# Performance work log

Hardware: AMD Instinct MI355X
Metric: run time of the kernel (lower is better)

The kernel has to match this reference:

```python
import jax, jax.numpy as jnp
import numpy as np

GAMMA, LMBD, EPS = 0.99, 0.95, 0.2
T, D, H, A = 262144, 128, 256, 8


def _mlp_gauss(x, W1, b1, Wmu, bmu, Wlv, blv):
    h = jnp.tanh(x @ W1 + b1)
    return h @ Wmu + bmu, h @ Wlv + blv  # mu, logvar: [T, A]


def _critic(x, Wc1, bc1, Wc2, bc2):
    h = jnp.tanh(x @ Wc1 + bc1)
    return h @ Wc2 + bc2  # [T, 1]


def setup_inputs() -> dict:
    key = jax.random.key(0)
    ks = jax.random.split(key, 12)
    s = 0.05  # small init scale for stable exp()/ratio
    return {
        "state": jax.random.normal(ks[0], (T, D), jnp.float32),
        "next_state": jax.random.normal(ks[1], (T, D), jnp.float32),
        "action": jax.random.normal(ks[2], (T, A), jnp.float32),
        "beta_log_prob": jax.random.normal(ks[3], (T, A), jnp.float32) * 0.1,
        "reward": jax.random.normal(ks[4], (T,), jnp.float32),
        "W1": jax.random.normal(ks[5], (D, H), jnp.float32) * s,
        "b1": jnp.zeros((H,), jnp.float32),
        "Wmu": jax.random.normal(ks[6], (H, A), jnp.float32) * s,
        "bmu": jnp.zeros((A,), jnp.float32),
        "Wlv": jax.random.normal(ks[7], (H, A), jnp.float32) * s,
        "blv": jnp.zeros((A,), jnp.float32),
        "Wc1": jax.random.normal(ks[8], (D, H), jnp.float32) * s,
        "bc1": jnp.zeros((H,), jnp.float32),
        "Wc2": jax.random.normal(ks[9], (H, 1), jnp.float32) * s,
        "bc2": jnp.zeros((1,), jnp.float32),
    }


def reference(state, next_state, action, beta_log_prob, reward,
              W1, b1, Wmu, bmu, Wlv, blv, Wc1, bc1, Wc2, bc2):
    # critic values
    value = _critic(state, Wc1, bc1, Wc2, bc2)            # [T, 1]
    v0 = value[:, 0]                                       # [T]
    v1 = _critic(next_state, Wc1, bc1, Wc2, bc2)[:, 0]     # [T]

    # GAE: reverse recurrence gae_t = delta_t + gamma*lambda*gae_{t+1}
    delta = reward + GAMMA * v1 - v0                       # [T]

    def step(g, d):
        g = d + GAMMA * LMBD * g
        return g, g

    _, gae_rev = jax.lax.scan(step, jnp.float32(0.0), delta[::-1])
    # torch code rebuilds each gae into a fresh Tensor -> returns are detached
    ret = jax.lax.stop_gradient(gae_rev[::-1][:, None])    # [T, 1]

    advantage = ret - value                                # [T, 1] (grad via value)
    a_hat = (advantage - advantage.mean()) / (jnp.std(advantage, ddof=1) + 1e-7)

    # pi log-prob of actions under Normal(mu, sqrt(exp(logvar)))
    mu, logvar = _mlp_gauss(state, W1, b1, Wmu, bmu, Wlv, blv)  # [T, A]
    log_2pi = jnp.float32(np.log(2.0 * np.pi))
    pi_lp = -0.5 * ((action - mu) ** 2) * jnp.exp(-logvar) - 0.5 * logvar - 0.5 * log_2pi

    ratio = jnp.exp(jnp.sum(pi_lp - jax.lax.stop_gradient(beta_log_prob),
                            axis=1, keepdims=True))        # [T, 1]

    actor_loss = -jnp.sum(jnp.minimum(ratio * a_hat,
                                      jnp.clip(ratio, 1.0 - EPS, 1.0 + EPS) * a_hat))
    critic_loss = jnp.sum(advantage ** 2)
    return actor_loss + critic_loss
```

## Files before the change

kernel.cpp:

```cpp
#include <hip/hip_runtime.h>

#define T_N   262144
#define D_IN  128
#define H_HID 256
#define A_DIM 8
#define GAMMA 0.99f
#define EPS_C 0.2f
#define C_GL  0.9405f
#define HALF_LOG_2PI 0.9189385332f

typedef __attribute__((ext_vector_type(8))) short short8;
typedef __attribute__((ext_vector_type(4))) float f32x4;

__device__ __forceinline__ unsigned short f2bf(float f) {
  unsigned int u = __float_as_uint(f);
  u += 0x7FFFu + ((u >> 16) & 1u);
  return (unsigned short)(u >> 16);
}
__device__ __forceinline__ float fast_tanh(float x) {
  x = fminf(10.f, fmaxf(-10.f, x));
  float e = __expf(2.f * x);
  return 1.f - 2.f * __builtin_amdgcn_rcpf(e + 1.f);
}

__global__ __launch_bounds__(256) void k_prep(
    const float* __restrict__ Wc1, const float* __restrict__ W1,
    const float* __restrict__ Wmu, const float* __restrict__ Wlv,
    unsigned short* __restrict__ Wc1T, unsigned short* __restrict__ W1T,
    unsigned short* __restrict__ H1) {
  int i = blockIdx.x * 256 + threadIdx.x;
  if (i < 32768) {
    int n = i >> 7, k = i & 127;
    Wc1T[i] = f2bf(Wc1[k * 256 + n]);
  } else if (i < 65536) {
    int j = i - 32768; int n = j >> 7, k = j & 127;
    W1T[j] = f2bf(W1[k * 256 + n]);
  } else if (i < 69632) {
    int j = i - 65536; int h = j >> 8, n = j & 255;
    H1[j] = (h < 8) ? f2bf(Wmu[n * 8 + h]) : f2bf(Wlv[n * 8 + (h - 8)]);
  }
}

__global__ __launch_bounds__(256, 4) void k_critic(
    const float* __restrict__ state, const float* __restrict__ next_state,
    const unsigned short* __restrict__ Wc1T,
    const float* __restrict__ bc1, const float* __restrict__ Wc2,
    const float* __restrict__ bc2,
    float* __restrict__ v0out, float* __restrict__ v1out) {
  const int job = blockIdx.y;
  const int r0  = blockIdx.x * 64;
  const int tid = threadIdx.x;
  const int lane = tid & 63;
  const int wv   = tid >> 6;
  const int c    = lane & 15;
  const int quad = lane >> 4;

  __shared__ unsigned short sh_x[64 * 136];
  __shared__ float sh_v[64 * 4];

  const float* X = job ? next_state : state;
  float* out = job ? v1out : v0out;

  {
    const float4* Xv = (const float4*)(X + r0 * D_IN);
#pragma unroll
    for (int it = 0; it < 8; ++it) {
      int f4 = tid + it * 256;
      int row = f4 >> 5, c4 = f4 & 31;
      float4 v = Xv[f4];
      ushort4 u;
      u.x = f2bf(v.x); u.y = f2bf(v.y); u.z = f2bf(v.z); u.w = f2bf(v.w);
      *(ushort4*)(&sh_x[row * 136 + c4 * 4]) = u;
    }
  }

  short8 bfrag[4][4];
  float bias_c[4], wc2_c[4];
#pragma unroll
  for (int ct = 0; ct < 4; ++ct) {
    int n = wv * 64 + ct * 16 + c;
    bias_c[ct] = bc1[n];
    wc2_c[ct]  = Wc2[n];
#pragma unroll
    for (int ki = 0; ki < 4; ++ki)
      bfrag[ct][ki] = *(const short8*)(Wc1T + n * 128 + ki * 32 + quad * 8);
  }
  __syncthreads();

#pragma unroll
  for (int rt = 0; rt < 4; ++rt) {
    f32x4 acc[4];
#pragma unroll
    for (int ct = 0; ct < 4; ++ct) acc[ct] = (f32x4){0.f, 0.f, 0.f, 0.f};
#pragma unroll
    for (int ki = 0; ki < 4; ++ki) {
      short8 a = *(const short8*)(&sh_x[(rt * 16 + c) * 136 + ki * 32 + quad * 8]);
#pragma unroll
      for (int ct = 0; ct < 4; ++ct)
        acc[ct] = __builtin_amdgcn_mfma_f32_16x16x32_bf16(a, bfrag[ct][ki], acc[ct], 0, 0, 0);
    }
#pragma unroll
    for (int r = 0; r < 4; ++r) {
      float p = 0.f;
#pragma unroll
      for (int ct = 0; ct < 4; ++ct)
        p += fast_tanh(acc[ct][r] + bias_c[ct]) * wc2_c[ct];
      p += __shfl_xor(p, 1);
      p += __shfl_xor(p, 2);
      p += __shfl_xor(p, 4);
      p += __shfl_xor(p, 8);
      if (c == 0) sh_v[(rt * 16 + quad * 4 + r) * 4 + wv] = p;
    }
  }
  __syncthreads();
  if (tid < 64) {
    out[r0 + tid] = sh_v[tid * 4] + sh_v[tid * 4 + 1] + sh_v[tid * 4 + 2] +
                    sh_v[tid * 4 + 3] + bc2[0];
  }
}

__global__ __launch_bounds__(256, 4) void k_actor(
    const float* __restrict__ state,
    const float* __restrict__ action, const float* __restrict__ beta_lp,
    const unsigned short* __restrict__ W1T, const unsigned short* __restrict__ H1,
    const float* __restrict__ b1, const float* __restrict__ bmu,
    const float* __restrict__ blv,
    float* __restrict__ ratio) {
  const int r0  = blockIdx.x * 32;
  const int tid = threadIdx.x;
  const int lane = tid & 63;
  const int wv   = tid >> 6;
  const int c    = lane & 15;
  const int quad = lane >> 4;

  __shared__ unsigned short sh_x[32 * 136];
  __shared__ unsigned short sh_h[32 * 264];
  __shared__ float sh_hb[2 * 32 * 16];

  {
    const float4* Xv = (const float4*)(state + r0 * D_IN);
#pragma unroll
    for (int it = 0; it < 4; ++it) {
      int f4 = tid + it * 256;
      int row = f4 >> 5, c4 = f4 & 31;
      float4 v = Xv[f4];
      ushort4 u;
      u.x = f2bf(v.x); u.y = f2bf(v.y); u.z = f2bf(v.z); u.w = f2bf(v.w);
      *(ushort4*)(&sh_x[row * 136 + c4 * 4]) = u;
    }
  }

  short8 bfrag[4][4];
  float bias_c[4];
#pragma unroll
  for (int ct = 0; ct < 4; ++ct) {
    int n = wv * 64 + ct * 16 + c;
    bias_c[ct] = b1[n];
#pragma unroll
    for (int ki = 0; ki < 4; ++ki)
      bfrag[ct][ki] = *(const short8*)(W1T + n * 128 + ki * 32 + quad * 8);
  }
  __syncthreads();

#pragma unroll
  for (int rt = 0; rt < 2; ++rt) {
    f32x4 acc[4];
#pragma unroll
    for (int ct = 0; ct < 4; ++ct) acc[ct] = (f32x4){0.f, 0.f, 0.f, 0.f};
#pragma unroll
    for (int ki = 0; ki < 4; ++ki) {
      short8 a = *(const short8*)(&sh_x[(rt * 16 + c) * 136 + ki * 32 + quad * 8]);
#pragma unroll
      for (int ct = 0; ct < 4; ++ct)
        acc[ct] = __builtin_amdgcn_mfma_f32_16x16x32_bf16(a, bfrag[ct][ki], acc[ct], 0, 0, 0);
    }
#pragma unroll
    for (int ct = 0; ct < 4; ++ct) {
      int col = wv * 64 + ct * 16 + c;
#pragma unroll
      for (int r = 0; r < 4; ++r) {
        int row = rt * 16 + quad * 4 + r;
        sh_h[row * 264 + col] = f2bf(fast_tanh(acc[ct][r] + bias_c[ct]));
      }
    }
  }
  __syncthreads();

  {
    const int st = wv & 1;
    const int kh = wv >> 1;
    f32x4 acc2 = (f32x4){0.f, 0.f, 0.f, 0.f};
#pragma unroll
    for (int kk = 0; kk < 4; ++kk) {
      int ki = kh * 4 + kk;
      short8 a2 = *(const short8*)(H1 + c * 256 + ki * 32 + quad * 8);
      short8 b2 = *(const short8*)(&sh_h[(st * 16 + c) * 264 + ki * 32 + quad * 8]);
      acc2 = __builtin_amdgcn_mfma_f32_16x16x32_bf16(a2, b2, acc2, 0, 0, 0);
    }
    *((f32x4*)&sh_hb[(kh * 32 + st * 16 + c) * 16 + quad * 4]) = acc2;
  }
  __syncthreads();

  {
    int s = tid >> 3, a = tid & 7;
    int t = r0 + s;
    float mu = sh_hb[(s)*16 + a] + sh_hb[(32 + s) * 16 + a] + bmu[a];
    float lv = sh_hb[(s)*16 + 8 + a] + sh_hb[(32 + s) * 16 + 8 + a] + blv[a];
    float ac = action[t * A_DIM + a];
    float bl = beta_lp[t * A_DIM + a];
    float d = ac - mu;
    float term = -0.5f * d * d * __expf(-lv) - 0.5f * lv - HALF_LOG_2PI - bl;
    term += __shfl_xor(term, 1);
    term += __shfl_xor(term, 2);
    term += __shfl_xor(term, 4);
    if (a == 0) ratio[t] = __expf(term);
  }
}

__global__ __launch_bounds__(256) void k_gae(
    const float* __restrict__ reward, const float* __restrict__ v0,
    const float* __restrict__ v1, float* __restrict__ adv,
    float* __restrict__ accs) {
  const int j = blockIdx.x, k = threadIdx.x;
  const int base = j * 1024 + k * 8;
  float d[8];
  float s = 0.f, w = 1.f;
#pragma unroll
  for (int i = 0; i < 8; ++i) {
    int idx = base + i;
    float dd = 0.f;
    if (idx < T_N) dd = reward[idx] + GAMMA * v1[idx] - v0[idx];
    d[i] = dd;
    s += w * dd;
    w *= C_GL;
  }
  const float W8 = w;
  __shared__ float Ss[256], Sw[256];
  Ss[k] = s; Sw[k] = W8;
  __syncthreads();
  for (int dd = 1; dd < 256; dd <<= 1) {
    bool has = (k + dd) < 256;
    float ns = 0.f, nw = 0.f;
    if (has) { ns = Ss[k] + Sw[k] * Ss[k + dd]; nw = Sw[k] * Sw[k + dd]; }
    __syncthreads();
    if (has) { Ss[k] = ns; Sw[k] = nw; }
    __syncthreads();
  }
  float g = (k < 255) ? Ss[k + 1] : 0.f;
  float sa = 0.f, sq = 0.f;
  if (k < 128) {
#pragma unroll
    for (int i = 7; i >= 0; --i) {
      g = d[i] + C_GL * g;
      float a = g - v0[base + i];
      adv[base + i] = a;
      sa += a; sq += a * a;
    }
  }
  __syncthreads();
  Ss[k] = sa; Sw[k] = sq;
  __syncthreads();
  for (int off = 128; off > 0; off >>= 1) {
    if (k < off) { Ss[k] += Ss[k + off]; Sw[k] += Sw[k + off]; }
    __syncthreads();
  }
  if (k == 0) {
    atomicAdd(&accs[0], Ss[0]);
    atomicAdd(&accs[1], Sw[0]);
  }
}

__global__ __launch_bounds__(256) void k_loss(
    const float* __restrict__ adv, const float* __restrict__ ratio,
    float* __restrict__ accs) {
  int t = blockIdx.x * 256 + threadIdx.x;
  float sum  = accs[0];
  float mean = sum * (1.f / (float)T_N);
  float var  = (accs[1] - sum * mean) / (float)(T_N - 1);
  float inv  = 1.f / (sqrtf(var) + 1e-7f);
  float a = (adv[t] - mean) * inv;
  float r = ratio[t];
  float rc = fminf(fmaxf(r, 1.f - EPS_C), 1.f + EPS_C);
  float term = -fminf(r * a, rc * a);
  __shared__ float red[256];
  int k = threadIdx.x;
  red[k] = term;
  __syncthreads();
  for (int off = 128; off > 0; off >>= 1) {
    if (k < off) red[k] += red[k + off];
    __syncthreads();
  }
  if (k == 0) atomicAdd(&accs[2], red[0]);
}

__global__ void k_fin(const float* __restrict__ accs, float* __restrict__ out) {
  out[0] = accs[2] + accs[1];
}

extern "C" void kernel_launch(void* const* d_in, const int* in_sizes, int n_in,
                              void* d_out, int out_size, void* d_ws, size_t ws_size,
                              hipStream_t stream) {
  const float* state      = (const float*)d_in[0];
  const float* next_state = (const float*)d_in[1];
  const float* action     = (const float*)d_in[2];
  const float* beta_lp    = (const float*)d_in[3];
  const float* reward     = (const float*)d_in[4];
  const float* W1   = (const float*)d_in[5];
  const float* b1   = (const float*)d_in[6];
  const float* Wmu  = (const float*)d_in[7];
  const float* bmu  = (const float*)d_in[8];
  const float* Wlv  = (const float*)d_in[9];
  const float* blv  = (const float*)d_in[10];
  const float* Wc1  = (const float*)d_in[11];
  const float* bc1  = (const float*)d_in[12];
  const float* Wc2  = (const float*)d_in[13];
  const float* bc2  = (const float*)d_in[14];

  char* ws = (char*)d_ws;
  size_t o = 0;
  unsigned short* Wc1T = (unsigned short*)(ws + o); o += 65536;
  unsigned short* W1T  = (unsigned short*)(ws + o); o += 65536;
  unsigned short* H1   = (unsigned short*)(ws + o); o += 8192;
  float* v0    = (float*)(ws + o); o += (size_t)T_N * 4;
  float* v1    = (float*)(ws + o); o += (size_t)T_N * 4;
  float* ratio = (float*)(ws + o); o += (size_t)T_N * 4;
  float* adv   = (float*)(ws + o); o += (size_t)T_N * 4;
  float* accs  = (float*)(ws + o); o += 256;

  hipMemsetAsync(accs, 0, 16, stream);

  k_prep<<<272, 256, 0, stream>>>(Wc1, W1, Wmu, Wlv, Wc1T, W1T, H1);

  dim3 gcrit(T_N / 64, 2);
  k_critic<<<gcrit, 256, 0, stream>>>(state, next_state, Wc1T, bc1, Wc2, bc2,
                                      v0, v1);
  k_actor<<<T_N / 32, 256, 0, stream>>>(state, action, beta_lp, W1T, H1,
                                        b1, bmu, blv, ratio);
  k_gae<<<256, 256, 0, stream>>>(reward, v0, v1, adv, accs);
  k_loss<<<T_N / 256, 256, 0, stream>>>(adv, ratio, accs);
  k_fin<<<1, 1, 0, stream>>>(accs, (float*)d_out);
}
```

Measured before the change: 440.4 us.

## Make critic/actor blocks persistent over multiple tiles with register prefetch; fold final kernel

Critic and actor kernels now loop over several 32-row tiles per block. Weight fragments are loaded into registers once per block, and the next tile's state rows are prefetched into registers while MFMA work runs on the current tile. The actor's second GEMM is split across all four waves by K, with a four-way partial-sum reduction. The separate finalize kernel is replaced by a last-block-done atomic counter inside k_loss. This cuts repeated weight loads and one launch, at the cost of fewer blocks and less parallelism across the grid.

```diff
diff --git a/kernel.cpp b/kernel.cpp
--- a/kernel.cpp
+++ b/kernel.cpp
@@ -8,6 +8,8 @@
 #define EPS_C 0.2f
 #define C_GL  0.9405f
 #define HALF_LOG_2PI 0.9189385332f
+#define CR_TPB 16
+#define AC_TPB 8
 
 typedef __attribute__((ext_vector_type(8))) short short8;
 typedef __attribute__((ext_vector_type(4))) float f32x4;
@@ -47,32 +49,14 @@
     const float* __restrict__ bc1, const float* __restrict__ Wc2,
     const float* __restrict__ bc2,
     float* __restrict__ v0out, float* __restrict__ v1out) {
-  const int job = blockIdx.y;
-  const int r0  = blockIdx.x * 64;
   const int tid = threadIdx.x;
   const int lane = tid & 63;
   const int wv   = tid >> 6;
   const int c    = lane & 15;
   const int quad = lane >> 4;
 
-  __shared__ unsigned short sh_x[64 * 136];
-  __shared__ float sh_v[64 * 4];
-
-  const float* X = job ? next_state : state;
-  float* out = job ? v1out : v0out;
-
-  {
-    const float4* Xv = (const float4*)(X + r0 * D_IN);
-#pragma unroll
-    for (int it = 0; it < 8; ++it) {
-      int f4 = tid + it * 256;
-      int row = f4 >> 5, c4 = f4 & 31;
-      float4 v = Xv[f4];
-      ushort4 u;
-      u.x = f2bf(v.x); u.y = f2bf(v.y); u.z = f2bf(v.z); u.w = f2bf(v.w);
-      *(ushort4*)(&sh_x[row * 136 + c4 * 4]) = u;
-    }
-  }
+  __shared__ unsigned short sh_x[32 * 136];
+  __shared__ float sh_v[32 * 4];
 
   short8 bfrag[4][4];
   float bias_c[4], wc2_c[4];
@@ -85,37 +69,73 @@
     for (int ki = 0; ki < 4; ++ki)
       bfrag[ct][ki] = *(const short8*)(Wc1T + n * 128 + ki * 32 + quad * 8);
   }
-  __syncthreads();
-
-#pragma unroll
-  for (int rt = 0; rt < 4; ++rt) {
-    f32x4 acc[4];
-#pragma unroll
-    for (int ct = 0; ct < 4; ++ct) acc[ct] = (f32x4){0.f, 0.f, 0.f, 0.f};
-#pragma unroll
-    for (int ki = 0; ki < 4; ++ki) {
-      short8 a = *(const short8*)(&sh_x[(rt * 16 + c) * 136 + ki * 32 + quad * 8]);
-#pragma unroll
-      for (int ct = 0; ct < 4; ++ct)
-        acc[ct] = __builtin_amdgcn_mfma_f32_16x16x32_bf16(a, bfrag[ct][ki], acc[ct], 0, 0, 0);
-    }
-#pragma unroll
-    for (int r = 0; r < 4; ++r) {
-      float p = 0.f;
-#pragma unroll
-      for (int ct = 0; ct < 4; ++ct)
-        p += fast_tanh(acc[ct][r] + bias_c[ct]) * wc2_c[ct];
-      p += __shfl_xor(p, 1);
-      p += __shfl_xor(p, 2);
-      p += __shfl_xor(p, 4);
-      p += __shfl_xor(p, 8);
-      if (c == 0) sh_v[(rt * 16 + quad * 4 + r) * 4 + wv] = p;
-    }
-  }
-  __syncthreads();
-  if (tid < 64) {
-    out[r0 + tid] = sh_v[tid * 4] + sh_v[tid * 4 + 1] + sh_v[tid * 4 + 2] +
-                    sh_v[tid * 4 + 3] + bc2[0];
+  const float vbias = bc2[0];
+
+  const int t0 = blockIdx.x * CR_TPB;
+
+  float4 rbuf[4];
+  {
+    const float* X = (t0 >> 13) ? next_state : state;
+    const float4* Xv = (const float4*)(X + (t0 & 8191) * 32 * D_IN);
+#pragma unroll
+    for (int j = 0; j < 4; ++j) rbuf[j] = Xv[tid + j * 256];
+  }
+
+  for (int i = 0; i < CR_TPB; ++i) {
+    const int T = t0 + i;
+    const int job = T >> 13;
+    const int r0  = (T & 8191) * 32;
+
+#pragma unroll
+    for (int j = 0; j < 4; ++j) {
+      int e = tid + j * 256;
+      int row = e >> 5, c4 = e & 31;
+      ushort4 u;
+      u.x = f2bf(rbuf[j].x); u.y = f2bf(rbuf[j].y);
+      u.z = f2bf(rbuf[j].z); u.w = f2bf(rbuf[j].w);
+      *(ushort4*)(&sh_x[row * 136 + c4 * 4]) = u;
+    }
+    __syncthreads();
+
+    if (i + 1 < CR_TPB) {
+      int T2 = T + 1;
+      const float* X2 = (T2 >> 13) ? next_state : state;
+      const float4* Xv2 = (const float4*)(X2 + (T2 & 8191) * 32 * D_IN);
+#pragma unroll
+      for (int j = 0; j < 4; ++j) rbuf[j] = Xv2[tid + j * 256];
+    }
+
+#pragma unroll
+    for (int rt = 0; rt < 2; ++rt) {
+      f32x4 acc[4];
+#pragma unroll
+      for (int ct = 0; ct < 4; ++ct) acc[ct] = (f32x4){0.f, 0.f, 0.f, 0.f};
+#pragma unroll
+      for (int ki = 0; ki < 4; ++ki) {
+        short8 a = *(const short8*)(&sh_x[(rt * 16 + c) * 136 + ki * 32 + quad * 8]);
+#pragma unroll
+        for (int ct = 0; ct < 4; ++ct)
+          acc[ct] = __builtin_amdgcn_mfma_f32_16x16x32_bf16(a, bfrag[ct][ki], acc[ct], 0, 0, 0);
+      }
+#pragma unroll
+      for (int r = 0; r < 4; ++r) {
+        float p = 0.f;
+#pragma unroll
+        for (int ct = 0; ct < 4; ++ct)
+          p += fast_tanh(acc[ct][r] + bias_c[ct]) * wc2_c[ct];
+        p += __shfl_xor(p, 1);
+        p += __shfl_xor(p, 2);
+        p += __shfl_xor(p, 4);
+        p += __shfl_xor(p, 8);
+        if (c == 0) sh_v[(rt * 16 + quad * 4 + r) * 4 + wv] = p;
+      }
+    }
+    __syncthreads();
+    if (tid < 32) {
+      float* out = job ? v1out : v0out;
+      out[r0 + tid] = sh_v[tid * 4] + sh_v[tid * 4 + 1] + sh_v[tid * 4 + 2] +
+                      sh_v[tid * 4 + 3] + vbias;
+    }
   }
 }
 
@@ -126,7 +146,6 @@
     const float* __restrict__ b1, const float* __restrict__ bmu,
     const float* __restrict__ blv,
     float* __restrict__ ratio) {
-  const int r0  = blockIdx.x * 32;
   const int tid = threadIdx.x;
   const int lane = tid & 63;
   const int wv   = tid >> 6;
@@ -135,20 +154,7 @@
 
   __shared__ unsigned short sh_x[32 * 136];
   __shared__ unsigned short sh_h[32 * 264];
-  __shared__ float sh_hb[2 * 32 * 16];
-
-  {
-    const float4* Xv = (const float4*)(state + r0 * D_IN);
-#pragma unroll
-    for (int it = 0; it < 4; ++it) {
-      int f4 = tid + it * 256;
-      int row = f4 >> 5, c4 = f4 & 31;
-      float4 v = Xv[f4];
-      ushort4 u;
-      u.x = f2bf(v.x); u.y = f2bf(v.y); u.z = f2bf(v.z); u.w = f2bf(v.w);
-      *(ushort4*)(&sh_x[row * 136 + c4 * 4]) = u;
-    }
-  }
+  __shared__ float sh_hb[4 * 32 * 16];
 
   short8 bfrag[4][4];
   float bias_c[4];
@@ -160,60 +166,92 @@
     for (int ki = 0; ki < 4; ++ki)
       bfrag[ct][ki] = *(const short8*)(W1T + n * 128 + ki * 32 + quad * 8);
   }
-  __syncthreads();
-
-#pragma unroll
-  for (int rt = 0; rt < 2; ++rt) {
-    f32x4 acc[4];
-#pragma unroll
-    for (int ct = 0; ct < 4; ++ct) acc[ct] = (f32x4){0.f, 0.f, 0.f, 0.f};
-#pragma unroll
-    for (int ki = 0; ki < 4; ++ki) {
-      short8 a = *(const short8*)(&sh_x[(rt * 16 + c) * 136 + ki * 32 + quad * 8]);
-#pragma unroll
-      for (int ct = 0; ct < 4; ++ct)
-        acc[ct] = __builtin_amdgcn_mfma_f32_16x16x32_bf16(a, bfrag[ct][ki], acc[ct], 0, 0, 0);
-    }
-#pragma unroll
-    for (int ct = 0; ct < 4; ++ct) {
-      int col = wv * 64 + ct * 16 + c;
-#pragma unroll
-      for (int r = 0; r < 4; ++r) {
-        int row = rt * 16 + quad * 4 + r;
-        sh_h[row * 264 + col] = f2bf(fast_tanh(acc[ct][r] + bias_c[ct]));
-      }
-    }
-  }
-  __syncthreads();
-
+  const int aa = tid & 7;
+  const float bmu_a = bmu[aa], blv_a = blv[aa];
+
+  const int t0 = blockIdx.x * AC_TPB;
+
+  float4 rbuf[4];
   {
-    const int st = wv & 1;
-    const int kh = wv >> 1;
-    f32x4 acc2 = (f32x4){0.f, 0.f, 0.f, 0.f};
-#pragma unroll
-    for (int kk = 0; kk < 4; ++kk) {
-      int ki = kh * 4 + kk;
-      short8 a2 = *(const short8*)(H1 + c * 256 + ki * 32 + quad * 8);
-      short8 b2 = *(const short8*)(&sh_h[(st * 16 + c) * 264 + ki * 32 + quad * 8]);
-      acc2 = __builtin_amdgcn_mfma_f32_16x16x32_bf16(a2, b2, acc2, 0, 0, 0);
-    }
-    *((f32x4*)&sh_hb[(kh * 32 + st * 16 + c) * 16 + quad * 4]) = acc2;
-  }
-  __syncthreads();
-
-  {
-    int s = tid >> 3, a = tid & 7;
-    int t = r0 + s;
-    float mu = sh_hb[(s)*16 + a] + sh_hb[(32 + s) * 16 + a] + bmu[a];
-    float lv = sh_hb[(s)*16 + 8 + a] + sh_hb[(32 + s) * 16 + 8 + a] + blv[a];
-    float ac = action[t * A_DIM + a];
-    float bl = beta_lp[t * A_DIM + a];
-    float d = ac - mu;
-    float term = -0.5f * d * d * __expf(-lv) - 0.5f * lv - HALF_LOG_2PI - bl;
-    term += __shfl_xor(term, 1);
-    term += __shfl_xor(term, 2);
-    term += __shfl_xor(term, 4);
-    if (a == 0) ratio[t] = __expf(term);
+    const float4* Xv = (const float4*)(state + t0 * 32 * D_IN);
+#pragma unroll
+    for (int j = 0; j < 4; ++j) rbuf[j] = Xv[tid + j * 256];
+  }
+
+  for (int i = 0; i < AC_TPB; ++i) {
+    const int r0 = (t0 + i) * 32;
+
+#pragma unroll
+    for (int j = 0; j < 4; ++j) {
+      int e = tid + j * 256;
+      int row = e >> 5, c4 = e & 31;
+      ushort4 u;
+      u.x = f2bf(rbuf[j].x); u.y = f2bf(rbuf[j].y);
+      u.z = f2bf(rbuf[j].z); u.w = f2bf(rbuf[j].w);
+      *(ushort4*)(&sh_x[row * 136 + c4 * 4]) = u;
+    }
+    __syncthreads();
+
+    if (i + 1 < AC_TPB) {
+      const float4* Xv2 = (const float4*)(state + (r0 + 32) * D_IN);
+#pragma unroll
+      for (int j = 0; j < 4; ++j) rbuf[j] = Xv2[tid + j * 256];
+    }
+
+#pragma unroll
+    for (int rt = 0; rt < 2; ++rt) {
+      f32x4 acc[4];
+#pragma unroll
+      for (int ct = 0; ct < 4; ++ct) acc[ct] = (f32x4){0.f, 0.f, 0.f, 0.f};
+#pragma unroll
+      for (int ki = 0; ki < 4; ++ki) {
+        short8 a = *(const short8*)(&sh_x[(rt * 16 + c) * 136 + ki * 32 + quad * 8]);
+#pragma unroll
+        for (int ct = 0; ct < 4; ++ct)
+          acc[ct] = __builtin_amdgcn_mfma_f32_16x16x32_bf16(a, bfrag[ct][ki], acc[ct], 0, 0, 0);
+      }
+#pragma unroll
+      for (int ct = 0; ct < 4; ++ct) {
+        int col = wv * 64 + ct * 16 + c;
+#pragma unroll
+        for (int r = 0; r < 4; ++r) {
+          int row = rt * 16 + quad * 4 + r;
+          sh_h[row * 264 + col] = f2bf(fast_tanh(acc[ct][r] + bias_c[ct]));
+        }
+      }
+    }
+    __syncthreads();
+
+#pragma unroll
+    for (int st = 0; st < 2; ++st) {
+      f32x4 acc2 = (f32x4){0.f, 0.f, 0.f, 0.f};
+#pragma unroll
+      for (int k2 = 0; k2 < 2; ++k2) {
+        int kofs = wv * 64 + k2 * 32 + quad * 8;
+        short8 a2 = *(const short8*)(H1 + c * 256 + kofs);
+        short8 b2 = *(const short8*)(&sh_h[(st * 16 + c) * 264 + kofs]);
+        acc2 = __builtin_amdgcn_mfma_f32_16x16x32_bf16(a2, b2, acc2, 0, 0, 0);
+      }
+      *((f32x4*)&sh_hb[((wv * 32) + st * 16 + c) * 16 + quad * 4]) = acc2;
+    }
+    __syncthreads();
+
+    {
+      int s = tid >> 3;
+      int t = r0 + s;
+      float mu = sh_hb[(s)*16 + aa]     + sh_hb[(32 + s) * 16 + aa] +
+                 sh_hb[(64 + s) * 16 + aa] + sh_hb[(96 + s) * 16 + aa] + bmu_a;
+      float lv = sh_hb[(s)*16 + 8 + aa]     + sh_hb[(32 + s) * 16 + 8 + aa] +
+                 sh_hb[(64 + s) * 16 + 8 + aa] + sh_hb[(96 + s) * 16 + 8 + aa] + blv_a;
+      float ac = action[t * A_DIM + aa];
+      float bl = beta_lp[t * A_DIM + aa];
+      float d = ac - mu;
+      float term = -0.5f * d * d * __expf(-lv) - 0.5f * lv - HALF_LOG_2PI - bl;
+      term += __shfl_xor(term, 1);
+      term += __shfl_xor(term, 2);
+      term += __shfl_xor(term, 4);
+      if (aa == 0) ratio[t] = __expf(term);
+    }
   }
 }
 
@@ -272,7 +310,7 @@
 
 __global__ __launch_bounds__(256) void k_loss(
     const float* __restrict__ adv, const float* __restrict__ ratio,
-    float* __restrict__ accs) {
+    float* __restrict__ accs, float* __restrict__ out) {
   int t = blockIdx.x * 256 + threadIdx.x;
   float sum  = accs[0];
   float mean = sum * (1.f / (float)T_N);
@@ -290,11 +328,16 @@
     if (k < off) red[k] += red[k + off];
     __syncthreads();
   }
-  if (k == 0) atomicAdd(&accs[2], red[0]);
-}
-
-__global__ void k_fin(const float* __restrict__ accs, float* __restrict__ out) {
-  out[0] = accs[2] + accs[1];
+  if (k == 0) {
+    atomicAdd(&accs[2], red[0]);
+    __threadfence();
+    unsigned int old = atomicAdd((unsigned int*)&accs[3], 1u);
+    if (old == (unsigned int)(gridDim.x - 1)) {
+      __threadfence();
+      volatile float* va = (volatile float*)accs;
+      out[0] = va[2] + va[1];
+    }
+  }
 }
 
 extern "C" void kernel_launch(void* const* d_in, const int* in_sizes, int n_in,
@@ -327,16 +370,14 @@
   float* adv   = (float*)(ws + o); o += (size_t)T_N * 4;
   float* accs  = (float*)(ws + o); o += 256;
 
-  hipMemsetAsync(accs, 0, 16, stream);
+  hipMemsetAsync(accs, 0, 32, stream);
 
   k_prep<<<272, 256, 0, stream>>>(Wc1, W1, Wmu, Wlv, Wc1T, W1T, H1);
 
-  dim3 gcrit(T_N / 64, 2);
-  k_critic<<<gcrit, 256, 0, stream>>>(state, next_state, Wc1T, bc1, Wc2, bc2,
-                                      v0, v1);
-  k_actor<<<T_N / 32, 256, 0, stream>>>(state, action, beta_lp, W1T, H1,
-                                        b1, bmu, blv, ratio);
+  k_critic<<<(2 * T_N / 32) / CR_TPB, 256, 0, stream>>>(
+      state, next_state, Wc1T, bc1, Wc2, bc2, v0, v1);
+  k_actor<<<(T_N / 32) / AC_TPB, 256, 0, stream>>>(
+      state, action, beta_lp, W1T, H1, b1, bmu, blv, ratio);
   k_gae<<<256, 256, 0, stream>>>(reward, v0, v1, adv, accs);
-  k_loss<<<T_N / 256, 256, 0, stream>>>(adv, ratio, accs);
-  k_fin<<<1, 1, 0, stream>>>(accs, (float*)d_out);
-}
+  k_loss<<<T_N / 256, 256, 0, stream>>>(adv, ratio, accs, (float*)d_out);
+}
```

Result: slower. 467.0 us (+6.0%).
